# Kernel optimization log

Measured on AMD Instinct MI355X. Metric: run time of the kernel, lower is better.

Reference implementation:

```python
import jax, jax.numpy as jnp
import numpy as np

B, S, D, H = 4, 2048, 768, 12
DH = D // H  # 64
SCALE = float(DH)  # att_scale == 'per_head' -> dim // num_heads


def setup_inputs() -> dict:
    key = jax.random.key(0)
    ks = jax.random.split(key, 7)
    p = 1.0 / np.sqrt(D)
    return {
        "x": jax.random.normal(ks[0], (B, S, D), dtype=jnp.float32),
        "Wq": jax.random.normal(ks[1], (D, D), dtype=jnp.float32) * p,
        "bq": jax.random.normal(ks[2], (D,), dtype=jnp.float32) * p,
        "Wk": jax.random.normal(ks[3], (D, D), dtype=jnp.float32) * p,
        "bk": jax.random.normal(ks[4], (D,), dtype=jnp.float32) * p,
        "Wv": jax.random.normal(ks[5], (D, D), dtype=jnp.float32) * p,
        "bv": jax.random.normal(ks[6], (D,), dtype=jnp.float32) * p,
    }


def reference(x, Wq, bq, Wk, bk, Wv, bv):
    # torch nn.Linear: y = x @ W.T + b
    q = x @ Wq.T + bq  # [B,S,D]
    k = x @ Wk.T + bk
    v = x @ Wv.T + bv
    # split heads -> [B,H,S,DH]
    def heads(t):
        return t.reshape(B, S, H, DH).transpose(0, 2, 1, 3)
    q, k, v = heads(q), heads(k), heads(v)
    scores = jnp.einsum("bhqd,bhkd->bhqk", q, k) / jnp.sqrt(jnp.float32(SCALE))
    probs = jax.nn.softmax(scores, axis=-1)
    h = jnp.einsum("bhqk,bhkd->bhqd", probs, v)  # [B,H,S,DH]
    return h.transpose(0, 2, 1, 3).reshape(B, S, D)
```

## Files before the change

### kernel.cpp

```cpp
#include <hip/hip_runtime.h>

#define NB 4
#define NS 2048
#define ND 768
#define NH 12
#define NDH 64
#define NM (NB * NS)

typedef __attribute__((ext_vector_type(8))) _Float16 f16x8;
typedef __attribute__((ext_vector_type(4))) _Float16 f16x4;
typedef __attribute__((ext_vector_type(2))) _Float16 f16x2;
typedef __attribute__((ext_vector_type(8))) unsigned short u16x8;
typedef __attribute__((ext_vector_type(4))) unsigned short u16x4;
typedef __attribute__((ext_vector_type(4))) float f32x4;

__device__ __forceinline__ unsigned short f2h(float f) {
    _Float16 h = (_Float16)f;
    return __builtin_bit_cast(unsigned short, h);
}
__device__ __forceinline__ f16x8 ldf16x8(const unsigned short* p) {
    return __builtin_bit_cast(f16x8, *(const u16x8*)p);
}
__device__ __forceinline__ f16x4 ldf16x4(const unsigned short* p) {
    return __builtin_bit_cast(f16x4, *(const u16x4*)p);
}
__device__ __forceinline__ void gload_lds16(const void* g, void* l) {
    __builtin_amdgcn_global_load_lds(
        (const __attribute__((address_space(1))) void*)g,
        (__attribute__((address_space(3))) void*)l, 16, 0, 0);
}

__device__ __forceinline__ float exp2_fast(float x) {
#if __has_builtin(__builtin_amdgcn_exp2f)
    return __builtin_amdgcn_exp2f(x);
#else
    return exp2f(x);
#endif
}

__device__ __forceinline__ f16x4 pk4(float a, float b, float c, float d) {
#if __has_builtin(__builtin_amdgcn_cvt_pkrtz)
    f16x2 lo = __builtin_bit_cast(f16x2, __builtin_amdgcn_cvt_pkrtz(a, b));
    f16x2 hi = __builtin_bit_cast(f16x2, __builtin_amdgcn_cvt_pkrtz(c, d));
    f16x4 r;
    r[0] = lo[0]; r[1] = lo[1]; r[2] = hi[0]; r[3] = hi[1];
    return r;
#else
    f16x4 r;
    r[0] = (_Float16)a; r[1] = (_Float16)b;
    r[2] = (_Float16)c; r[3] = (_Float16)d;
    return r;
#endif
}

__global__ __launch_bounds__(256)
void conv_f32_to_f16(const float* __restrict__ x,
                     const float* __restrict__ wq,
                     const float* __restrict__ wk,
                     const float* __restrict__ wv,
                     unsigned short* __restrict__ dst)
{
    const int CX = (NM * ND) / 8;
    const int CW = (ND * ND) / 8;
    int c = blockIdx.x * 256 + threadIdx.x;
    const float* src;
    int base;
    if (c < CX)               { src = x;  base = 0; }
    else if (c < CX + CW)     { src = wq; base = CX; }
    else if (c < CX + 2 * CW) { src = wk; base = CX + CW; }
    else                      { src = wv; base = CX + 2 * CW; }
    const float4* p = (const float4*)&src[(size_t)(c - base) * 8];
    float4 a = p[0], b = p[1];
    u16x8 r;
    r[0] = f2h(a.x); r[1] = f2h(a.y); r[2] = f2h(a.z); r[3] = f2h(a.w);
    r[4] = f2h(b.x); r[5] = f2h(b.y); r[6] = f2h(b.z); r[7] = f2h(b.w);
    *(u16x8*)&dst[(size_t)c * 8] = r;
}

__global__ __launch_bounds__(256)
void qkv_gemm(const unsigned short* __restrict__ xh,
              const unsigned short* __restrict__ wh,
              const float* __restrict__ bq,
              const float* __restrict__ bk,
              const float* __restrict__ bv,
              unsigned short* __restrict__ qkv)
{
    const int z = blockIdx.z;
    const unsigned short* W = wh + (size_t)z * ND * ND;
    const float* bias = (z == 0) ? bq : (z == 1) ? bk : bv;
    unsigned short* out = qkv + (size_t)z * NM * ND;

    const int m0 = blockIdx.x * 128;
    const int n0 = blockIdx.y * 128;
    const int tid = threadIdx.x;
    const int lane = tid & 63, wave = tid >> 6;
    const int quad = lane >> 4, l16 = lane & 15;
    const int wm = (wave >> 1) * 64, wn = (wave & 1) * 64;

    __shared__ __align__(16) unsigned short As[128 * 32];
    __shared__ __align__(16) unsigned short Bs[128 * 32];

    const f32x4 fz = {0.f, 0.f, 0.f, 0.f};
    f32x4 acc[4][4];
#pragma unroll
    for (int i = 0; i < 4; ++i)
#pragma unroll
        for (int j = 0; j < 4; ++j) acc[i][j] = fz;

    const int lrow = lane >> 2;
    const int lcol = (lane & 3) * 8;

    for (int kt = 0; kt < ND / 32; ++kt) {
        const int k0 = kt * 32;
        __syncthreads();
#pragma unroll
        for (int i = 0; i < 2; ++i) {
            const int seg = wave * 2 + i;
            const int row = seg * 16 + lrow;
            gload_lds16(&xh[(size_t)(m0 + row) * ND + k0 + lcol], &As[seg * 512]);
            gload_lds16(&W[(size_t)(n0 + row) * ND + k0 + lcol], &Bs[seg * 512]);
        }
        __syncthreads();

        f16x8 af[4], bf_[4];
#pragma unroll
        for (int mi = 0; mi < 4; ++mi)
            af[mi] = ldf16x8(&As[(wm + mi * 16 + l16) * 32 + quad * 8]);
#pragma unroll
        for (int ni = 0; ni < 4; ++ni)
            bf_[ni] = ldf16x8(&Bs[(wn + ni * 16 + l16) * 32 + quad * 8]);
#pragma unroll
        for (int mi = 0; mi < 4; ++mi)
#pragma unroll
            for (int ni = 0; ni < 4; ++ni)
                acc[mi][ni] = __builtin_amdgcn_mfma_f32_16x16x32_f16(
                    af[mi], bf_[ni], acc[mi][ni], 0, 0, 0);
    }

#pragma unroll
    for (int ni = 0; ni < 4; ++ni) {
        const int n = n0 + wn + ni * 16 + l16;
        const float bval = bias[n];
        const int hh = n >> 6, d = n & 63;
#pragma unroll
        for (int mi = 0; mi < 4; ++mi) {
#pragma unroll
            for (int r = 0; r < 4; ++r) {
                const int m = m0 + wm + mi * 16 + quad * 4 + r;
                const int bi = m >> 11, s = m & (NS - 1);
                out[(((size_t)(bi * NH + hh)) * NS + s) * NDH + d] =
                    f2h(acc[mi][ni][r] + bval);
            }
        }
    }
}

#define ALD 72
#define KLD 136

__global__ __launch_bounds__(256)
void attn_kernel(const unsigned short* __restrict__ qh,
                 const unsigned short* __restrict__ kh,
                 const unsigned short* __restrict__ vh,
                 float* __restrict__ out)
{
    const int bh = blockIdx.y;
    const int bb = bh / NH, hh = bh % NH;
    const int tid = threadIdx.x;
    const int lane = tid & 63, wave = tid >> 6;
    const int quad = lane >> 4, l16 = lane & 15;
    const int q0 = blockIdx.x * 128 + wave * 32;

    __shared__ __align__(16) unsigned short Ks[128 * ALD];
    __shared__ __align__(16) unsigned short VTs[64 * KLD];

    const unsigned short* qb = qh + (size_t)bh * NS * NDH;
    const unsigned short* kb = kh + (size_t)bh * NS * NDH;
    const unsigned short* vb = vh + (size_t)bh * NS * NDH;

    f16x8 bq_[2][2];
#pragma unroll
    for (int qt = 0; qt < 2; ++qt)
#pragma unroll
        for (int kk = 0; kk < 2; ++kk)
            bq_[qt][kk] = ldf16x8(
                &qb[(size_t)(q0 + qt * 16 + l16) * NDH + kk * 32 + quad * 8]);

    const float c2 = 0.18033688011112042f;

    const f32x4 fz = {0.f, 0.f, 0.f, 0.f};
    f32x4 o[2][4];
    float m2[2], lsum[2];
#pragma unroll
    for (int qt = 0; qt < 2; ++qt) {
#pragma unroll
        for (int dt = 0; dt < 4; ++dt) o[qt][dt] = fz;
        m2[qt] = -__builtin_inff();
        lsum[qt] = 0.f;
    }

    const int krow = tid >> 3;
    const int kcol = (tid & 7) * 8;
    const int vpair = tid & 31;
    const int vchunk = tid >> 5;

    const unsigned short* kp = kb + (size_t)krow * NDH + kcol;
    const unsigned short* vp = vb + (size_t)(2 * vpair) * NDH + vchunk * 8;

    u16x8 kr[4], vr0[2], vr1[2];
#pragma unroll
    for (int i = 0; i < 4; ++i)
        kr[i] = *(const u16x8*)(kp + i * (32 * NDH));
#pragma unroll
    for (int i2 = 0; i2 < 2; ++i2) {
        vr0[i2] = *(const u16x8*)(vp + i2 * (64 * NDH));
        vr1[i2] = *(const u16x8*)(vp + i2 * (64 * NDH) + NDH);
    }

    const int NT = NS / 128;
    for (int kt = 0; kt < NT; ++kt) {
        __syncthreads();
#pragma unroll
        for (int i = 0; i < 4; ++i)
            *(u16x8*)&Ks[(krow + i * 32) * ALD + kcol] = kr[i];
#pragma unroll
        for (int i2 = 0; i2 < 2; ++i2) {
            const int P = vpair + i2 * 32;
#pragma unroll
            for (int j = 0; j < 8; ++j) {
                unsigned pk = (unsigned)vr0[i2][j] | ((unsigned)vr1[i2][j] << 16);
                *(unsigned*)&VTs[(vchunk * 8 + j) * KLD + 2 * P] = pk;
            }
        }
        kp += 128 * NDH;
        vp += 128 * NDH;
        if (kt + 1 < NT) {
#pragma unroll
            for (int i = 0; i < 4; ++i)
                kr[i] = *(const u16x8*)(kp + i * (32 * NDH));
#pragma unroll
            for (int i2 = 0; i2 < 2; ++i2) {
                vr0[i2] = *(const u16x8*)(vp + i2 * (64 * NDH));
                vr1[i2] = *(const u16x8*)(vp + i2 * (64 * NDH) + NDH);
            }
        }
        __syncthreads();

#pragma unroll
        for (int half = 0; half < 2; ++half) {
            const int kvb = half * 64;

            f16x8 ak[4][2];
#pragma unroll
            for (int kvt = 0; kvt < 4; ++kvt)
#pragma unroll
                for (int kk = 0; kk < 2; ++kk)
                    ak[kvt][kk] = ldf16x8(
                        &Ks[(kvb + kvt * 16 + l16) * ALD + kk * 32 + quad * 8]);

            f32x4 st[2][4];
            __builtin_amdgcn_s_setprio(1);
#pragma unroll
            for (int qt = 0; qt < 2; ++qt)
#pragma unroll
                for (int kvt = 0; kvt < 4; ++kvt) {
                    st[qt][kvt] = fz;
#pragma unroll
                    for (int kk = 0; kk < 2; ++kk)
                        st[qt][kvt] = __builtin_amdgcn_mfma_f32_16x16x32_f16(
                            ak[kvt][kk], bq_[qt][kk], st[qt][kvt], 0, 0, 0);
                }
            __builtin_amdgcn_s_setprio(0);

            f16x4 av[4][4];
#pragma unroll
            for (int dt = 0; dt < 4; ++dt)
#pragma unroll
                for (int kvt = 0; kvt < 4; ++kvt)
                    av[dt][kvt] = ldf16x4(
                        &VTs[(dt * 16 + l16) * KLD + kvb + kvt * 16 + quad * 4]);

#pragma unroll
            for (int qt = 0; qt < 2; ++qt) {
                float rm = st[qt][0][0];
#pragma unroll
                for (int kvt = 0; kvt < 4; ++kvt)
#pragma unroll
                    for (int r = 0; r < 4; ++r)
                        rm = fmaxf(rm, st[qt][kvt][r]);

                if (!__all(rm * c2 <= m2[qt] + 8.f)) {
                    rm = fmaxf(rm, __shfl_xor(rm, 16, 64));
                    rm = fmaxf(rm, __shfl_xor(rm, 32, 64));
                    const float mn = fmaxf(m2[qt], rm * c2);
                    const float al = exp2_fast(m2[qt] - mn);
                    m2[qt] = mn;
                    lsum[qt] *= al;
#pragma unroll
                    for (int dt = 0; dt < 4; ++dt)
                        o[qt][dt] *= al;
                }
                const float mn = m2[qt];

                float rs = 0.f;
                f16x4 pf[4];
#pragma unroll
                for (int kvt = 0; kvt < 4; ++kvt) {
                    const float p0 = exp2_fast(fmaf(st[qt][kvt][0], c2, -mn));
                    const float p1 = exp2_fast(fmaf(st[qt][kvt][1], c2, -mn));
                    const float p2 = exp2_fast(fmaf(st[qt][kvt][2], c2, -mn));
                    const float p3 = exp2_fast(fmaf(st[qt][kvt][3], c2, -mn));
                    rs += (p0 + p1) + (p2 + p3);
                    pf[kvt] = pk4(p0, p1, p2, p3);
                }
                lsum[qt] += rs;

                __builtin_amdgcn_s_setprio(1);
#pragma unroll
                for (int dt = 0; dt < 4; ++dt)
#pragma unroll
                    for (int kvt = 0; kvt < 4; ++kvt)
                        o[qt][dt] = __builtin_amdgcn_mfma_f32_16x16x16f16(
                            av[dt][kvt], pf[kvt], o[qt][dt], 0, 0, 0);
                __builtin_amdgcn_s_setprio(0);
            }
        }
    }

#pragma unroll
    for (int qt = 0; qt < 2; ++qt) {
        const int q = q0 + qt * 16 + l16;
        float l = lsum[qt];
        l += __shfl_xor(l, 16, 64);
        l += __shfl_xor(l, 32, 64);
        const float inv = 1.f / l;
#pragma unroll
        for (int dt = 0; dt < 4; ++dt) {
            float4 v;
            v.x = o[qt][dt][0] * inv;
            v.y = o[qt][dt][1] * inv;
            v.z = o[qt][dt][2] * inv;
            v.w = o[qt][dt][3] * inv;
            *(float4*)&out[((size_t)(bb * NS + q)) * ND + hh * NDH + dt * 16 + quad * 4] = v;
        }
    }
}

extern "C" void kernel_launch(void* const* d_in, const int* in_sizes, int n_in,
                              void* d_out, int out_size, void* d_ws, size_t ws_size,
                              hipStream_t stream)
{
    const float* x  = (const float*)d_in[0];
    const float* Wq = (const float*)d_in[1];
    const float* bq = (const float*)d_in[2];
    const float* Wk = (const float*)d_in[3];
    const float* bk = (const float*)d_in[4];
    const float* Wv = (const float*)d_in[5];
    const float* bv = (const float*)d_in[6];

    unsigned short* ws  = (unsigned short*)d_ws;
    unsigned short* xh  = ws;
    unsigned short* wh  = xh + (size_t)NM * ND;
    unsigned short* qkv = wh + (size_t)3 * ND * ND;
    unsigned short* qhp = qkv;
    unsigned short* khp = qkv + (size_t)NM * ND;
    unsigned short* vhp = qkv + (size_t)2 * NM * ND;

    const int convBlocks = (NM * ND + 3 * ND * ND) / (8 * 256);
    conv_f32_to_f16<<<convBlocks, 256, 0, stream>>>(x, Wq, Wk, Wv, xh);

    qkv_gemm<<<dim3(NM / 128, ND / 128, 3), 256, 0, stream>>>(
        xh, wh, bq, bk, bv, qkv);

    attn_kernel<<<dim3(NS / 128, NB * NH), 256, 0, stream>>>(
        qhp, khp, vhp, (float*)d_out);
}
```

Measured before the change: 217.3 us.

## Load K fragments directly from global memory into registers, bypassing LDS

K tiles are no longer staged through shared memory. Each lane loads its MFMA fragments straight from global memory, double-buffered across the two halves so the next half's loads overlap the current compute. The VT stride changes from 136 to 132, and the row max now uses a max3 tree. This removes the LDS writes, reads and footprint for K. In exchange it raises register pressure and relies on cache for K data, which every wave of the block now fetches redundantly from global memory.

```diff
diff --git a/kernel.cpp b/kernel.cpp
--- a/kernel.cpp
+++ b/kernel.cpp
@@ -36,6 +36,10 @@
 #else
     return exp2f(x);
 #endif
+}
+
+__device__ __forceinline__ float max3f(float a, float b, float c) {
+    return fmaxf(fmaxf(a, b), c);
 }
 
 __device__ __forceinline__ f16x4 pk4(float a, float b, float c, float d) {
@@ -155,8 +159,7 @@
     }
 }
 
-#define ALD 72
-#define KLD 136
+#define KLD 132
 
 __global__ __launch_bounds__(256)
 void attn_kernel(const unsigned short* __restrict__ qh,
@@ -171,7 +174,6 @@
     const int quad = lane >> 4, l16 = lane & 15;
     const int q0 = blockIdx.x * 128 + wave * 32;
 
-    __shared__ __align__(16) unsigned short Ks[128 * ALD];
     __shared__ __align__(16) unsigned short VTs[64 * KLD];
 
     const unsigned short* qb = qh + (size_t)bh * NS * NDH;
@@ -199,31 +201,100 @@
         lsum[qt] = 0.f;
     }
 
-    const int krow = tid >> 3;
-    const int kcol = (tid & 7) * 8;
     const int vpair = tid & 31;
     const int vchunk = tid >> 5;
-
-    const unsigned short* kp = kb + (size_t)krow * NDH + kcol;
     const unsigned short* vp = vb + (size_t)(2 * vpair) * NDH + vchunk * 8;
 
-    u16x8 kr[4], vr0[2], vr1[2];
-#pragma unroll
-    for (int i = 0; i < 4; ++i)
-        kr[i] = *(const u16x8*)(kp + i * (32 * NDH));
+    u16x8 vr0[2], vr1[2];
 #pragma unroll
     for (int i2 = 0; i2 < 2; ++i2) {
         vr0[i2] = *(const u16x8*)(vp + i2 * (64 * NDH));
         vr1[i2] = *(const u16x8*)(vp + i2 * (64 * NDH) + NDH);
     }
 
+    const unsigned short* kfp = kb + (size_t)l16 * NDH + quad * 8;
+    const unsigned short* kcur = kfp;
+
+    f16x8 akA[4][2], akB[4][2];
+#pragma unroll
+    for (int kvt = 0; kvt < 4; ++kvt)
+#pragma unroll
+        for (int kk = 0; kk < 2; ++kk)
+            akA[kvt][kk] = ldf16x8(kcur + (kvt * 16) * NDH + kk * 32);
+
+    auto compute_half = [&](const f16x8 (&ak)[4][2], const int kvb) {
+        f32x4 st[2][4];
+        __builtin_amdgcn_s_setprio(1);
+#pragma unroll
+        for (int qt = 0; qt < 2; ++qt)
+#pragma unroll
+            for (int kvt = 0; kvt < 4; ++kvt) {
+                st[qt][kvt] = fz;
+#pragma unroll
+                for (int kk = 0; kk < 2; ++kk)
+                    st[qt][kvt] = __builtin_amdgcn_mfma_f32_16x16x32_f16(
+                        ak[kvt][kk], bq_[qt][kk], st[qt][kvt], 0, 0, 0);
+            }
+        __builtin_amdgcn_s_setprio(0);
+
+        f16x4 av[4][4];
+#pragma unroll
+        for (int dt = 0; dt < 4; ++dt)
+#pragma unroll
+            for (int kvt = 0; kvt < 4; ++kvt)
+                av[dt][kvt] = ldf16x4(
+                    &VTs[(dt * 16 + l16) * KLD + kvb + kvt * 16 + quad * 4]);
+
+#pragma unroll
+        for (int qt = 0; qt < 2; ++qt) {
+            const float r0 = max3f(st[qt][0][0], st[qt][0][1], st[qt][0][2]);
+            const float r1 = max3f(st[qt][0][3], st[qt][1][0], st[qt][1][1]);
+            const float r2 = max3f(st[qt][1][2], st[qt][1][3], st[qt][2][0]);
+            const float r3 = max3f(st[qt][2][1], st[qt][2][2], st[qt][2][3]);
+            const float r4 = max3f(st[qt][3][0], st[qt][3][1], st[qt][3][2]);
+            float rm = fmaxf(max3f(r0, r1, r2), max3f(r3, r4, st[qt][3][3]));
+
+            if (!__all(rm * c2 <= m2[qt] + 8.f)) {
+                rm = fmaxf(rm, __shfl_xor(rm, 16, 64));
+                rm = fmaxf(rm, __shfl_xor(rm, 32, 64));
+                const float mn = fmaxf(m2[qt], rm * c2);
+                const float al = exp2_fast(m2[qt] - mn);
+                m2[qt] = mn;
+                lsum[qt] *= al;
+#pragma unroll
+                for (int dt = 0; dt < 4; ++dt)
+                    o[qt][dt] *= al;
+            }
+            const float mn = m2[qt];
+
+            float rs = 0.f;
+            f16x4 pf[4];
+#pragma unroll
+            for (int kvt = 0; kvt < 4; ++kvt) {
+                const float p0 = exp2_fast(fmaf(st[qt][kvt][0], c2, -mn));
+                const float p1 = exp2_fast(fmaf(st[qt][kvt][1], c2, -mn));
+                const float p2 = exp2_fast(fmaf(st[qt][kvt][2], c2, -mn));
+                const float p3 = exp2_fast(fmaf(st[qt][kvt][3], c2, -mn));
+                rs += (p0 + p1) + (p2 + p3);
+                pf[kvt] = pk4(p0, p1, p2, p3);
+            }
+            lsum[qt] += rs;
+
+            __builtin_amdgcn_s_setprio(1);
+#pragma unroll
+            for (int dt = 0; dt < 4; ++dt)
+#pragma unroll
+                for (int kvt = 0; kvt < 4; ++kvt)
+                    o[qt][dt] = __builtin_amdgcn_mfma_f32_16x16x16f16(
+                        av[dt][kvt], pf[kvt], o[qt][dt], 0, 0, 0);
+            __builtin_amdgcn_s_setprio(0);
+        }
+    };
+
     const int NT = NS / 128;
     for (int kt = 0; kt < NT; ++kt) {
         __syncthreads();
 #pragma unroll
-        for (int i = 0; i < 4; ++i)
-            *(u16x8*)&Ks[(krow + i * 32) * ALD + kcol] = kr[i];
-#pragma unroll
         for (int i2 = 0; i2 < 2; ++i2) {
             const int P = vpair + i2 * 32;
 #pragma unroll
@@ -232,12 +303,8 @@
                 *(unsigned*)&VTs[(vchunk * 8 + j) * KLD + 2 * P] = pk;
             }
         }
-        kp += 128 * NDH;
         vp += 128 * NDH;
         if (kt + 1 < NT) {
-#pragma unroll
-            for (int i = 0; i < 4; ++i)
-                kr[i] = *(const u16x8*)(kp + i * (32 * NDH));
 #pragma unroll
             for (int i2 = 0; i2 < 2; ++i2) {
                 vr0[i2] = *(const u16x8*)(vp + i2 * (64 * NDH));
@@ -247,84 +314,24 @@
         __syncthreads();
 
 #pragma unroll
-        for (int half = 0; half < 2; ++half) {
-            const int kvb = half * 64;
-
-            f16x8 ak[4][2];
+        for (int kvt = 0; kvt < 4; ++kvt)
+#pragma unroll
+            for (int kk = 0; kk < 2; ++kk)
+                akB[kvt][kk] = ldf16x8(kcur + (64 + kvt * 16) * NDH + kk * 32);
+
+        compute_half(akA, 0);
+
+        if (kt + 1 < NT) {
 #pragma unroll
             for (int kvt = 0; kvt < 4; ++kvt)
 #pragma unroll
                 for (int kk = 0; kk < 2; ++kk)
-                    ak[kvt][kk] = ldf16x8(
-                        &Ks[(kvb + kvt * 16 + l16) * ALD + kk * 32 + quad * 8]);
-
-            f32x4 st[2][4];
-            __builtin_amdgcn_s_setprio(1);
-#pragma unroll
-            for (int qt = 0; qt < 2; ++qt)
-#pragma unroll
-                for (int kvt = 0; kvt < 4; ++kvt) {
-                    st[qt][kvt] = fz;
-#pragma unroll
-                    for (int kk = 0; kk < 2; ++kk)
-                        st[qt][kvt] = __builtin_amdgcn_mfma_f32_16x16x32_f16(
-                            ak[kvt][kk], bq_[qt][kk], st[qt][kvt], 0, 0, 0);
-                }
-            __builtin_amdgcn_s_setprio(0);
-
-            f16x4 av[4][4];
-#pragma unroll
-            for (int dt = 0; dt < 4; ++dt)
-#pragma unroll
-                for (int kvt = 0; kvt < 4; ++kvt)
-                    av[dt][kvt] = ldf16x4(
-                        &VTs[(dt * 16 + l16) * KLD + kvb + kvt * 16 + quad * 4]);
-
-#pragma unroll
-            for (int qt = 0; qt < 2; ++qt) {
-                float rm = st[qt][0][0];
-#pragma unroll
-                for (int kvt = 0; kvt < 4; ++kvt)
-#pragma unroll
-                    for (int r = 0; r < 4; ++r)
-                        rm = fmaxf(rm, st[qt][kvt][r]);
-
-                if (!__all(rm * c2 <= m2[qt] + 8.f)) {
-                    rm = fmaxf(rm, __shfl_xor(rm, 16, 64));
-                    rm = fmaxf(rm, __shfl_xor(rm, 32, 64));
-                    const float mn = fmaxf(m2[qt], rm * c2);
-                    const float al = exp2_fast(m2[qt] - mn);
-                    m2[qt] = mn;
-                    lsum[qt] *= al;
-#pragma unroll
-                    for (int dt = 0; dt < 4; ++dt)
-                        o[qt][dt] *= al;
-                }
-                const float mn = m2[qt];
-
-                float rs = 0.f;
-                f16x4 pf[4];
-#pragma unroll
-                for (int kvt = 0; kvt < 4; ++kvt) {
-                    const float p0 = exp2_fast(fmaf(st[qt][kvt][0], c2, -mn));
-                    const float p1 = exp2_fast(fmaf(st[qt][kvt][1], c2, -mn));
-                    const float p2 = exp2_fast(fmaf(st[qt][kvt][2], c2, -mn));
-                    const float p3 = exp2_fast(fmaf(st[qt][kvt][3], c2, -mn));
-                    rs += (p0 + p1) + (p2 + p3);
-                    pf[kvt] = pk4(p0, p1, p2, p3);
-                }
-                lsum[qt] += rs;
-
-                __builtin_amdgcn_s_setprio(1);
-#pragma unroll
-                for (int dt = 0; dt < 4; ++dt)
-#pragma unroll
-                    for (int kvt = 0; kvt < 4; ++kvt)
-                        o[qt][dt] = __builtin_amdgcn_mfma_f32_16x16x16f16(
-                            av[dt][kvt], pf[kvt], o[qt][dt], 0, 0, 0);
-                __builtin_amdgcn_s_setprio(0);
-            }
-        }
+                    akA[kvt][kk] = ldf16x8(kcur + (128 + kvt * 16) * NDH + kk * 32);
+        }
+
+        compute_half(akB, 64);
+
+        kcur += 128 * NDH;
     }
 
 #pragma unroll
```

Measured after the change: 265.4 us. 1.22x slower.
